# Kernel tuning notes

Hardware: AMD Instinct MI355X
Metric: run time of the kernel (lower is better)

## Reference

```python
import jax, jax.numpy as jnp
import numpy as np

B, L, D = 8, 2048, 64


def setup_inputs() -> dict:
    key = jax.random.key(0)
    kq, kk, kv = jax.random.split(key, 3)
    query = jax.random.normal(kq, (B, L, D), dtype=jnp.float32)
    key_t = jax.random.normal(kk, (B, L, D), dtype=jnp.float32)
    value = jax.random.normal(kv, (B, L, D), dtype=jnp.float32)
    return {"query": query, "key": key_t, "value": value}


def reference(query, key, value):
    d = query.shape[-1]
    # e = Q K^T / sqrt(d_k)   -> [B, Lq, Lk]
    scale = 1.0 / np.sqrt(float(d)).astype(np.float32)
    e = jnp.einsum("bqd,bkd->bqk", query, key) * scale
    # stable softmax over keys (matches exp(e - max)/sum in source)
    attention = jax.nn.softmax(e, axis=-1)
    # v = A V   -> [B, Lq, Dv]
    return jnp.einsum("bqk,bkd->bqd", attention, value)
```

## Files before the change

### kernel.cpp

```cpp
#include <hip/hip_runtime.h>


#define B_ 8
#define L_ 2048
#define D_ 64
#define NT 256
#define PS 40
#define KPW 512
#define TK 32

typedef _Float16 half8_t __attribute__((ext_vector_type(8)));
typedef float f32x4 __attribute__((ext_vector_type(4)));

__global__ __launch_bounds__(NT) void prepass(
    const float* __restrict__ Q, const float* __restrict__ K,
    const float* __restrict__ V,
    _Float16* __restrict__ Q16, _Float16* __restrict__ K16,
    _Float16* __restrict__ VT16)
{
    const int blk = blockIdx.x;
    const int t = threadIdx.x;
    if (blk < 1024) {
        const float* src = (blk < 512) ? Q : K;
        _Float16* dst    = (blk < 512) ? Q16 : K16;
        const int i = (blk & 511) * NT + t;
        const float4* s4 = (const float4*)src;
        const float4 a = s4[2 * i], b = s4[2 * i + 1];
        half8_t w;
        w[0] = (_Float16)a.x; w[1] = (_Float16)a.y;
        w[2] = (_Float16)a.z; w[3] = (_Float16)a.w;
        w[4] = (_Float16)b.x; w[5] = (_Float16)b.y;
        w[6] = (_Float16)b.z; w[7] = (_Float16)b.w;
        ((half8_t*)dst)[i] = w;
    } else {
        __shared__ __align__(16) _Float16 Lt[64 * 72];
        const int bb = (blk - 1024) >> 5;
        const int kt = (blk - 1024) & 31;
        const int r  = t >> 2;
        const int ch = t & 3;
        const float* vrow = V + ((size_t)bb * L_ + kt * 64 + r) * D_ + ch * 16;
        #pragma unroll
        for (int i = 0; i < 4; ++i) {
            const float4 f = ((const float4*)vrow)[i];
            const int d0 = ch * 16 + i * 4;
            Lt[(d0 + 0) * 72 + r] = (_Float16)f.x;
            Lt[(d0 + 1) * 72 + r] = (_Float16)f.y;
            Lt[(d0 + 2) * 72 + r] = (_Float16)f.z;
            Lt[(d0 + 3) * 72 + r] = (_Float16)f.w;
        }
        __syncthreads();
        const int d  = t >> 2;
        const int c2 = t & 3;
        const half8_t w0 = *(const half8_t*)&Lt[d * 72 + c2 * 16];
        const half8_t w1 = *(const half8_t*)&Lt[d * 72 + c2 * 16 + 8];
        _Float16* orow = VT16 + ((size_t)bb * D_ + d) * L_ + kt * 64 + c2 * 16;
        *(half8_t*)orow = w0;
        *(half8_t*)(orow + 8) = w1;
    }
}

__global__ __launch_bounds__(NT) void attn_split(
    const _Float16* __restrict__ Q16,
    const _Float16* __restrict__ K16,
    const _Float16* __restrict__ VT16,
    float* __restrict__ O)
{
    __shared__ __align__(16) unsigned char pool[34304];

    const int t    = threadIdx.x;
    const int wave = t >> 6;
    const int lane = t & 63;
    const int quad = lane >> 4;
    const int l15  = lane & 15;

    const int b  = blockIdx.x & 7;
    const int qb = (blockIdx.x >> 3) * 32;
    const int key0 = wave * KPW;

    _Float16* Pt   = (_Float16*)pool + wave * 32 * PS;
    float*    Ored = (float*)pool;
    float*    Lred = (float*)(pool + 33792);

    const _Float16* Qb = Q16 + ((size_t)b * L_ + qb) * D_;
    const _Float16* Kb = K16 + (size_t)b * L_ * D_;
    const _Float16* Vb = VT16 + (size_t)b * D_ * L_;

    half8_t aq[2][2];
    #pragma unroll
    for (int qs = 0; qs < 2; ++qs)
        #pragma unroll
        for (int c = 0; c < 2; ++c)
            aq[qs][c] = *(const half8_t*)&Qb[(size_t)(qs * 16 + l15) * D_ + c * 32 + quad * 8];

    f32x4 ofr[2][4];
    #pragma unroll
    for (int qs = 0; qs < 2; ++qs)
        #pragma unroll
        for (int d = 0; d < 4; ++d)
            ofr[qs][d] = (f32x4){0.f, 0.f, 0.f, 0.f};
    float lacc[2][4] = {{0.f, 0.f, 0.f, 0.f}, {0.f, 0.f, 0.f, 0.f}};

    for (int kt = 0; kt < KPW / TK; ++kt) {
        const int kbase = key0 + kt * TK;

        half8_t bk[2][2];
        #pragma unroll
        for (int s = 0; s < 2; ++s)
            #pragma unroll
            for (int c = 0; c < 2; ++c)
                bk[s][c] = *(const half8_t*)&Kb[(size_t)(kbase + s * 16 + l15) * D_ + c * 32 + quad * 8];

        f32x4 sc[2][2];
        #pragma unroll
        for (int qs = 0; qs < 2; ++qs)
            #pragma unroll
            for (int s = 0; s < 2; ++s) {
                f32x4 acc = (f32x4){0.f, 0.f, 0.f, 0.f};
                acc = __builtin_amdgcn_mfma_f32_16x16x32_f16(aq[qs][0], bk[s][0], acc, 0, 0, 0);
                acc = __builtin_amdgcn_mfma_f32_16x16x32_f16(aq[qs][1], bk[s][1], acc, 0, 0, 0);
                sc[qs][s] = acc;
            }

        #pragma unroll
        for (int qs = 0; qs < 2; ++qs)
            #pragma unroll
            for (int s = 0; s < 2; ++s)
                #pragma unroll
                for (int r = 0; r < 4; ++r) {
                    const float p = __expf(sc[qs][s][r] * 0.125f);
                    lacc[qs][r] += p;
                    Pt[(qs * 16 + quad * 4 + r) * PS + s * 16 + l15] = (_Float16)p;
                }

        __builtin_amdgcn_wave_barrier();

        half8_t bv[4];
        #pragma unroll
        for (int d = 0; d < 4; ++d)
            bv[d] = *(const half8_t*)&Vb[(size_t)(d * 16 + l15) * L_ + kbase + quad * 8];
        half8_t ap[2];
        #pragma unroll
        for (int qs = 0; qs < 2; ++qs)
            ap[qs] = *(const half8_t*)&Pt[(qs * 16 + l15) * PS + quad * 8];

        #pragma unroll
        for (int qs = 0; qs < 2; ++qs)
            #pragma unroll
            for (int d = 0; d < 4; ++d)
                ofr[qs][d] = __builtin_amdgcn_mfma_f32_16x16x32_f16(ap[qs], bv[d], ofr[qs][d], 0, 0, 0);

        __builtin_amdgcn_wave_barrier();
    }

    #pragma unroll
    for (int qs = 0; qs < 2; ++qs)
        #pragma unroll
        for (int r = 0; r < 4; ++r) {
            float v = lacc[qs][r];
            v += __shfl_xor(v, 1, 64);
            v += __shfl_xor(v, 2, 64);
            v += __shfl_xor(v, 4, 64);
            v += __shfl_xor(v, 8, 64);
            lacc[qs][r] = v;
        }

    __syncthreads();

    #pragma unroll
    for (int qs = 0; qs < 2; ++qs)
        #pragma unroll
        for (int d = 0; d < 4; ++d)
            #pragma unroll
            for (int r = 0; r < 4; ++r)
                Ored[(wave * 64 + lane) * 33 + qs * 16 + d * 4 + r] = ofr[qs][d][r];
    if (l15 == 0) {
        #pragma unroll
        for (int qs = 0; qs < 2; ++qs)
            #pragma unroll
            for (int r = 0; r < 4; ++r)
                Lred[wave * 32 + qs * 16 + quad * 4 + r] = lacc[qs][r];
    }
    __syncthreads();

    #pragma unroll
    for (int qs = 0; qs < 2; ++qs)
        #pragma unroll
        for (int r = 0; r < 4; ++r) {
            float osum = 0.f;
            #pragma unroll
            for (int w2 = 0; w2 < 4; ++w2)
                osum += Ored[(w2 * 64 + lane) * 33 + qs * 16 + wave * 4 + r];
            const int row = qs * 16 + quad * 4 + r;
            const float lt = Lred[row] + Lred[32 + row] + Lred[64 + row] + Lred[96 + row];
            O[((size_t)b * L_ + qb + row) * D_ + wave * 16 + l15] = osum / lt;
        }
}

#define KS 72
__global__ __launch_bounds__(NT) void attn_mfma_f16(
    const float* __restrict__ Q, const float* __restrict__ K,
    const float* __restrict__ V, float* __restrict__ O)
{
    __shared__ __align__(16) _Float16 Kt[64 * KS];
    __shared__ __align__(16) _Float16 Vt[D_ * KS];
    __shared__ __align__(16) _Float16 Pt[4][16 * KS];

    const int t = threadIdx.x;
    const int wave = t >> 6, lane = t & 63, quad = lane >> 4, l15 = lane & 15;
    const int bpb = L_ / 64;
    const int b = blockIdx.x / bpb;
    const int qb = (blockIdx.x % bpb) * 64 + wave * 16;
    const size_t boff = (size_t)b * L_ * D_;

    half8_t aq[2];
    {
        const float* qp = Q + boff + (size_t)(qb + l15) * D_ + quad * 8;
        #pragma unroll
        for (int c = 0; c < 2; ++c) {
            const float4* p4 = (const float4*)(qp + c * 32);
            const float4 f0 = p4[0], f1 = p4[1];
            aq[c][0] = (_Float16)f0.x; aq[c][1] = (_Float16)f0.y;
            aq[c][2] = (_Float16)f0.z; aq[c][3] = (_Float16)f0.w;
            aq[c][4] = (_Float16)f1.x; aq[c][5] = (_Float16)f1.y;
            aq[c][6] = (_Float16)f1.z; aq[c][7] = (_Float16)f1.w;
        }
    }
    f32x4 ofr[4];
    #pragma unroll
    for (int d = 0; d < 4; ++d) ofr[d] = (f32x4){0.f, 0.f, 0.f, 0.f};
    float lacc[4] = {0.f, 0.f, 0.f, 0.f};
    const int skey = t & 63, sdg = t >> 6;
    _Float16* Pw = &Pt[wave][0];

    for (int kt = 0; kt < L_ / 64; ++kt) {
        __syncthreads();
        {
            const float4* kg4 = (const float4*)(K + boff + (size_t)(kt * 64 + skey) * D_ + sdg * 16);
            const float4 f0 = kg4[0], f1 = kg4[1], f2 = kg4[2], f3 = kg4[3];
            half8_t w0, w1;
            w0[0] = (_Float16)f0.x; w0[1] = (_Float16)f0.y;
            w0[2] = (_Float16)f0.z; w0[3] = (_Float16)f0.w;
            w0[4] = (_Float16)f1.x; w0[5] = (_Float16)f1.y;
            w0[6] = (_Float16)f1.z; w0[7] = (_Float16)f1.w;
            w1[0] = (_Float16)f2.x; w1[1] = (_Float16)f2.y;
            w1[2] = (_Float16)f2.z; w1[3] = (_Float16)f2.w;
            w1[4] = (_Float16)f3.x; w1[5] = (_Float16)f3.y;
            w1[6] = (_Float16)f3.z; w1[7] = (_Float16)f3.w;
            *(half8_t*)&Kt[skey * KS + sdg * 16] = w0;
            *(half8_t*)&Kt[skey * KS + sdg * 16 + 8] = w1;
        }
        {
            const float4* vg4 = (const float4*)(V + boff + (size_t)(kt * 64 + skey) * D_ + sdg * 16);
            #pragma unroll
            for (int i = 0; i < 4; ++i) {
                const float4 f = vg4[i];
                const int d0 = sdg * 16 + i * 4;
                Vt[(d0 + 0) * KS + skey] = (_Float16)f.x;
                Vt[(d0 + 1) * KS + skey] = (_Float16)f.y;
                Vt[(d0 + 2) * KS + skey] = (_Float16)f.z;
                Vt[(d0 + 3) * KS + skey] = (_Float16)f.w;
            }
        }
        __syncthreads();
        #pragma unroll
        for (int s = 0; s < 4; ++s) {
            const half8_t bk0 = *(const half8_t*)&Kt[(s * 16 + l15) * KS + quad * 8];
            const half8_t bk1 = *(const half8_t*)&Kt[(s * 16 + l15) * KS + 32 + quad * 8];
            f32x4 sc = (f32x4){0.f, 0.f, 0.f, 0.f};
            sc = __builtin_amdgcn_mfma_f32_16x16x32_f16(aq[0], bk0, sc, 0, 0, 0);
            sc = __builtin_amdgcn_mfma_f32_16x16x32_f16(aq[1], bk1, sc, 0, 0, 0);
            #pragma unroll
            for (int r = 0; r < 4; ++r) {
                const float p = __expf(sc[r] * 0.125f);
                lacc[r] += p;
                Pw[(quad * 4 + r) * KS + s * 16 + l15] = (_Float16)p;
            }
        }
        __syncthreads();
        #pragma unroll
        for (int c = 0; c < 2; ++c) {
            const half8_t ap = *(const half8_t*)&Pw[l15 * KS + c * 32 + quad * 8];
            #pragma unroll
            for (int d = 0; d < 4; ++d) {
                const half8_t bv = *(const half8_t*)&Vt[(d * 16 + l15) * KS + c * 32 + quad * 8];
                ofr[d] = __builtin_amdgcn_mfma_f32_16x16x32_f16(ap, bv, ofr[d], 0, 0, 0);
            }
        }
    }
    #pragma unroll
    for (int r = 0; r < 4; ++r) {
        float v = lacc[r];
        v += __shfl_xor(v, 1, 64);
        v += __shfl_xor(v, 2, 64);
        v += __shfl_xor(v, 4, 64);
        v += __shfl_xor(v, 8, 64);
        lacc[r] = v;
    }
    #pragma unroll
    for (int r = 0; r < 4; ++r) {
        const float inv = 1.0f / lacc[r];
        float* orow = O + boff + (size_t)(qb + quad * 4 + r) * D_ + l15;
        #pragma unroll
        for (int d = 0; d < 4; ++d) orow[d * 16] = ofr[d][r] * inv;
    }
}

extern "C" void kernel_launch(void* const* d_in, const int* in_sizes, int n_in,
                              void* d_out, int out_size, void* d_ws, size_t ws_size,
                              hipStream_t stream) {
    const float* Q = (const float*)d_in[0];
    const float* K = (const float*)d_in[1];
    const float* V = (const float*)d_in[2];
    float* O = (float*)d_out;

    if (ws_size >= 3u * 2097152u) {
        _Float16* Q16  = (_Float16*)d_ws;
        _Float16* K16  = Q16 + 1048576;
        _Float16* VT16 = K16 + 1048576;
        prepass<<<1280, NT, 0, stream>>>(Q, K, V, Q16, K16, VT16);
        attn_split<<<512, NT, 0, stream>>>(Q16, K16, VT16, O);
    } else {
        attn_mfma_f16<<<256, NT, 0, stream>>>(Q, K, V, O);
    }
}
```

Before: 98.42 us.

## Split keys across two blocks with partial outputs and add combine kernel

Attention now splits the key dimension across two blocks per query tile (1024 blocks instead of 512), writing unnormalized partial outputs and row sums to workspace, and a new combine kernel adds the two halves and normalizes. Q conversion to fp16 moves from the prepass into the attention kernel, with the scale and log2(e) folded into Q so the softmax uses exp2 directly. V loads are hoisted before the score MFMAs, and launch bounds now request higher occupancy. The aim is more parallelism and less prepass traffic, at the cost of an extra kernel launch and partial-result round trips through memory.

New measurement: 106.4 us. +8.1%, slower.

```diff
diff --git a/kernel.cpp b/kernel.cpp
--- a/kernel.cpp
+++ b/kernel.cpp
@@ -6,36 +6,34 @@
 #define D_ 64
 #define NT 256
 #define PS 40
-#define KPW 512
 #define TK 32
 
 typedef _Float16 half8_t __attribute__((ext_vector_type(8)));
 typedef float f32x4 __attribute__((ext_vector_type(4)));
 
+#define SCALE_LOG2E 0.1803368801111244f
+
 __global__ __launch_bounds__(NT) void prepass(
-    const float* __restrict__ Q, const float* __restrict__ K,
-    const float* __restrict__ V,
-    _Float16* __restrict__ Q16, _Float16* __restrict__ K16,
-    _Float16* __restrict__ VT16)
+    const float* __restrict__ K, const float* __restrict__ V,
+    _Float16* __restrict__ K16, _Float16* __restrict__ VT16)
 {
     const int blk = blockIdx.x;
     const int t = threadIdx.x;
-    if (blk < 1024) {
-        const float* src = (blk < 512) ? Q : K;
-        _Float16* dst    = (blk < 512) ? Q16 : K16;
-        const int i = (blk & 511) * NT + t;
-        const float4* s4 = (const float4*)src;
+    if (blk < 512) {
+        const int i = blk * NT + t;
+        const float4* s4 = (const float4*)K;
         const float4 a = s4[2 * i], b = s4[2 * i + 1];
         half8_t w;
         w[0] = (_Float16)a.x; w[1] = (_Float16)a.y;
         w[2] = (_Float16)a.z; w[3] = (_Float16)a.w;
         w[4] = (_Float16)b.x; w[5] = (_Float16)b.y;
         w[6] = (_Float16)b.z; w[7] = (_Float16)b.w;
-        ((half8_t*)dst)[i] = w;
+        ((half8_t*)K16)[i] = w;
     } else {
         __shared__ __align__(16) _Float16 Lt[64 * 72];
-        const int bb = (blk - 1024) >> 5;
-        const int kt = (blk - 1024) & 31;
+        const int vblk = blk - 512;
+        const int bb = vblk >> 5;
+        const int kt = vblk & 31;
         const int r  = t >> 2;
         const int ch = t & 3;
         const float* vrow = V + ((size_t)bb * L_ + kt * 64 + r) * D_ + ch * 16;
@@ -59,11 +57,12 @@
     }
 }
 
-__global__ __launch_bounds__(NT) void attn_split(
-    const _Float16* __restrict__ Q16,
+__global__ __launch_bounds__(NT, 4) void attn_part(
+    const float* __restrict__ Q,
     const _Float16* __restrict__ K16,
     const _Float16* __restrict__ VT16,
-    float* __restrict__ O)
+    float* __restrict__ Opart,
+    float* __restrict__ lpart)
 {
     __shared__ __align__(16) unsigned char pool[34304];
 
@@ -73,24 +72,37 @@
     const int quad = lane >> 4;
     const int l15  = lane & 15;
 
-    const int b  = blockIdx.x & 7;
-    const int qb = (blockIdx.x >> 3) * 32;
-    const int key0 = wave * KPW;
+    const int b   = blockIdx.x & 7;
+    const int ks  = (blockIdx.x >> 3) & 1;
+    const int qbi = blockIdx.x >> 4;
+    const int qb  = qbi * 32;
+    const int key0 = ks * 1024 + wave * 256;
 
     _Float16* Pt   = (_Float16*)pool + wave * 32 * PS;
     float*    Ored = (float*)pool;
     float*    Lred = (float*)(pool + 33792);
 
-    const _Float16* Qb = Q16 + ((size_t)b * L_ + qb) * D_;
     const _Float16* Kb = K16 + (size_t)b * L_ * D_;
     const _Float16* Vb = VT16 + (size_t)b * D_ * L_;
 
     half8_t aq[2][2];
     #pragma unroll
-    for (int qs = 0; qs < 2; ++qs)
-        #pragma unroll
-        for (int c = 0; c < 2; ++c)
-            aq[qs][c] = *(const half8_t*)&Qb[(size_t)(qs * 16 + l15) * D_ + c * 32 + quad * 8];
+    for (int qs = 0; qs < 2; ++qs) {
+        const float* qp = Q + ((size_t)b * L_ + qb + qs * 16 + l15) * D_ + quad * 8;
+        #pragma unroll
+        for (int c = 0; c < 2; ++c) {
+            const float4 f0 = *(const float4*)(qp + c * 32);
+            const float4 f1 = *(const float4*)(qp + c * 32 + 4);
+            aq[qs][c][0] = (_Float16)(f0.x * SCALE_LOG2E);
+            aq[qs][c][1] = (_Float16)(f0.y * SCALE_LOG2E);
+            aq[qs][c][2] = (_Float16)(f0.z * SCALE_LOG2E);
+            aq[qs][c][3] = (_Float16)(f0.w * SCALE_LOG2E);
+            aq[qs][c][4] = (_Float16)(f1.x * SCALE_LOG2E);
+            aq[qs][c][5] = (_Float16)(f1.y * SCALE_LOG2E);
+            aq[qs][c][6] = (_Float16)(f1.z * SCALE_LOG2E);
+            aq[qs][c][7] = (_Float16)(f1.w * SCALE_LOG2E);
+        }
+    }
 
     f32x4 ofr[2][4];
     #pragma unroll
@@ -100,7 +112,7 @@
             ofr[qs][d] = (f32x4){0.f, 0.f, 0.f, 0.f};
     float lacc[2][4] = {{0.f, 0.f, 0.f, 0.f}, {0.f, 0.f, 0.f, 0.f}};
 
-    for (int kt = 0; kt < KPW / TK; ++kt) {
+    for (int kt = 0; kt < 256 / TK; ++kt) {
         const int kbase = key0 + kt * TK;
 
         half8_t bk[2][2];
@@ -109,6 +121,10 @@
             #pragma unroll
             for (int c = 0; c < 2; ++c)
                 bk[s][c] = *(const half8_t*)&Kb[(size_t)(kbase + s * 16 + l15) * D_ + c * 32 + quad * 8];
+        half8_t bv[4];
+        #pragma unroll
+        for (int d = 0; d < 4; ++d)
+            bv[d] = *(const half8_t*)&Vb[(size_t)(d * 16 + l15) * L_ + kbase + quad * 8];
 
         f32x4 sc[2][2];
         #pragma unroll
@@ -127,17 +143,13 @@
             for (int s = 0; s < 2; ++s)
                 #pragma unroll
                 for (int r = 0; r < 4; ++r) {
-                    const float p = __expf(sc[qs][s][r] * 0.125f);
+                    const float p = __builtin_exp2f(sc[qs][s][r]);
                     lacc[qs][r] += p;
                     Pt[(qs * 16 + quad * 4 + r) * PS + s * 16 + l15] = (_Float16)p;
                 }
 
         __builtin_amdgcn_wave_barrier();
 
-        half8_t bv[4];
-        #pragma unroll
-        for (int d = 0; d < 4; ++d)
-            bv[d] = *(const half8_t*)&Vb[(size_t)(d * 16 + l15) * L_ + kbase + quad * 8];
         half8_t ap[2];
         #pragma unroll
         for (int qs = 0; qs < 2; ++qs)
@@ -182,6 +194,9 @@
     }
     __syncthreads();
 
+    const size_t pidx  = (size_t)(b * 64 + qbi) * 2 + ks;
+    float* ob = Opart + pidx * 2048;
+    float* lb = lpart + pidx * 32;
     #pragma unroll
     for (int qs = 0; qs < 2; ++qs)
         #pragma unroll
@@ -191,9 +206,35 @@
             for (int w2 = 0; w2 < 4; ++w2)
                 osum += Ored[(w2 * 64 + lane) * 33 + qs * 16 + wave * 4 + r];
             const int row = qs * 16 + quad * 4 + r;
-            const float lt = Lred[row] + Lred[32 + row] + Lred[64 + row] + Lred[96 + row];
-            O[((size_t)b * L_ + qb + row) * D_ + wave * 16 + l15] = osum / lt;
-        }
+            ob[row * 64 + wave * 16 + l15] = osum;
+            if (wave == 0 && l15 == 0)
+                lb[row] = Lred[row] + Lred[32 + row] + Lred[64 + row] + Lred[96 + row];
+        }
+}
+
+__global__ __launch_bounds__(NT) void combine(
+    const float* __restrict__ Opart, const float* __restrict__ lpart,
+    float* __restrict__ O)
+{
+    const int blk = blockIdx.x;
+    const int t = threadIdx.x;
+    const float4* p0 = (const float4*)(Opart + (size_t)blk * 2 * 2048);
+    const float4* p1 = p0 + 512;
+    const float* l0 = lpart + (size_t)blk * 2 * 32;
+    const float* l1 = l0 + 32;
+    float4* out = (float4*)(O + (size_t)blk * 2048);
+    #pragma unroll
+    for (int i = 0; i < 2; ++i) {
+        const int idx = i * NT + t;
+        const int q = idx >> 4;
+        const float inv = 1.0f / (l0[q] + l1[q]);
+        const float4 a = p0[idx];
+        const float4 b = p1[idx];
+        float4 r;
+        r.x = (a.x + b.x) * inv; r.y = (a.y + b.y) * inv;
+        r.z = (a.z + b.z) * inv; r.w = (a.w + b.w) * inv;
+        out[idx] = r;
+    }
 }
 
 #define KS 72
@@ -313,12 +354,14 @@
     const float* V = (const float*)d_in[2];
     float* O = (float*)d_out;
 
-    if (ws_size >= 3u * 2097152u) {
-        _Float16* Q16  = (_Float16*)d_ws;
-        _Float16* K16  = Q16 + 1048576;
+    if (ws_size >= (size_t)16 * 1024 * 1024) {
+        _Float16* K16  = (_Float16*)d_ws;
         _Float16* VT16 = K16 + 1048576;
-        prepass<<<1280, NT, 0, stream>>>(Q, K, V, Q16, K16, VT16);
-        attn_split<<<512, NT, 0, stream>>>(Q16, K16, VT16, O);
+        float* Opart = (float*)((char*)d_ws + 4 * 1024 * 1024);
+        float* lpart = (float*)((char*)d_ws + 12 * 1024 * 1024);
+        prepass<<<768, NT, 0, stream>>>(K, V, K16, VT16);
+        attn_part<<<1024, NT, 0, stream>>>(Q, K16, VT16, Opart, lpart);
+        combine<<<512, NT, 0, stream>>>(Opart, lpart, O);
     } else {
         attn_mfma_f16<<<256, NT, 0, stream>>>(Q, K, V, O);
     }
```
